# Kernel tuning notes

Hardware: AMD Instinct MI355X
Metric: run time of the kernel (lower is better)

## Reference

```python
import jax, jax.numpy as jnp
import numpy as np
from jax import lax

EPS = 1e-08


def setup_inputs() -> dict:
    key = jax.random.key(0)
    kX, kY, kXs, kW, kA, kB1, kB2 = jax.random.split(key, 7)
    P, D, K, M = 8192, 1024, 131072, 512
    return {
        "X": jax.random.normal(kX, (P, D), dtype=jnp.float32),
        "y": jax.random.normal(kY, (P,), dtype=jnp.float32),
        "X_star": jax.random.normal(kXs, (K, D), dtype=jnp.float32),
        "gamma": jnp.float32(0.001),
        "W": jax.random.normal(kW, (M, D), dtype=jnp.float32) * 0.01,
        "a": jax.random.normal(kA, (M,), dtype=jnp.float32) * 0.01,
        "b1": jax.random.normal(kB1, (M,), dtype=jnp.float32) * 0.01,
        "b2": jnp.float32(0.1),
        "L": 64,
    }


def reference(X, y, X_star, gamma, W, a, b1, b2, L):
    P, D = X.shape
    Sigma_hat = (X.T @ X) / P                      # (D, D)
    I = jnp.eye(D, dtype=X.dtype)
    M_mat = I - (gamma / L) * Sigma_hat            # (D, D)

    # S = sum_{l=0}^{L-1} M^l, built sequentially as in the original loop
    def step(carry, _):
        S, Mp = carry
        return (S + Mp, Mp @ M_mat), None

    (S, _), _ = lax.scan(step, (jnp.zeros_like(I), I), None, length=L)

    rep = gamma * (S @ (X.T @ y))                  # (D,)
    linear_pred = (X_star @ rep) / (L * P)         # (K,)

    rep_normalized = rep / (jnp.linalg.norm(rep) + EPS)
    phi = X_star * rep_normalized                  # (K, D) elementwise
    hidden = jax.nn.relu(phi @ W.T + b1)           # (K, m)
    mlp_correction = hidden @ a                    # (K,)
    return linear_pred + mlp_correction + b2
```

## Files before the change

kernel.cpp:

```cpp
#include <hip/hip_runtime.h>
#include <hip/hip_bf16.h>
#include <stdint.h>

#define D_DIM 1024
#define P_ROWS 8192
#define K_ROWS 131072
#define M_DIM 512
#define L_STEPS 64
#define BM 128
#define XS_ROW_BYTES 4096

typedef short bf16x8_t __attribute__((ext_vector_type(8)));
typedef float f32x4_t __attribute__((ext_vector_type(4)));

typedef const __attribute__((address_space(1))) void* gas_t;
typedef __attribute__((address_space(3))) void* las_t;

__device__ __forceinline__ uint32_t f2bf(float f) {
  union { float f; uint32_t u; } c; c.f = f;
  const uint32_t u = c.u;
  return (u + 0x7FFFu + ((u >> 16) & 1u)) >> 16;
}

__device__ __forceinline__ bf16x8_t as_bf16x8(uint4 v) {
  union { uint4 u; bf16x8_t h; } c; c.u = v; return c.h;
}

__device__ __forceinline__ bf16x8_t cvt_frag(const f32x4_t& a0, const f32x4_t& a1) {
  uint32_t p0, p1, p2, p3;
  asm("v_cvt_pk_bf16_f32 %0, %1, %2" : "=v"(p0) : "v"(a0[0]), "v"(a0[1]));
  asm("v_cvt_pk_bf16_f32 %0, %1, %2" : "=v"(p1) : "v"(a0[2]), "v"(a0[3]));
  asm("v_cvt_pk_bf16_f32 %0, %1, %2" : "=v"(p2) : "v"(a1[0]), "v"(a1[1]));
  asm("v_cvt_pk_bf16_f32 %0, %1, %2" : "=v"(p3) : "v"(a1[2]), "v"(a1[3]));
  union { uint32_t u[4]; bf16x8_t h; } c;
  c.u[0] = p0; c.u[1] = p1; c.u[2] = p2; c.u[3] = p3;
  return c.h;
}

__global__ void xty_kernel(const float* __restrict__ X, const float* __restrict__ y,
                           float* __restrict__ v) {
  const int d0 = threadIdx.x * 4;
  float a0 = 0.f, a1 = 0.f, a2 = 0.f, a3 = 0.f;
  for (int i = blockIdx.x; i < P_ROWS; i += gridDim.x) {
    const float s = y[i];
    const float4 x = *reinterpret_cast<const float4*>(X + (size_t)i * D_DIM + d0);
    a0 += s * x.x; a1 += s * x.y; a2 += s * x.z; a3 += s * x.w;
  }
  atomicAdd(v + d0 + 0, a0);
  atomicAdd(v + d0 + 1, a1);
  atomicAdd(v + d0 + 2, a2);
  atomicAdd(v + d0 + 3, a3);
}

__global__ void xtxw_kernel(const float* __restrict__ X, const float* __restrict__ win,
                            float* __restrict__ wout) {
  __shared__ float red[4][D_DIM];
  const int lane = threadIdx.x & 63;
  const int wave = threadIdx.x >> 6;
  const int gw = blockIdx.x * 4 + wave;
  const int nw = gridDim.x * 4;
  float wv[16], acc[16];
#pragma unroll
  for (int q = 0; q < 4; ++q) {
    const float4 tv = *reinterpret_cast<const float4*>(win + q * 256 + lane * 4);
    wv[q*4+0] = tv.x; wv[q*4+1] = tv.y; wv[q*4+2] = tv.z; wv[q*4+3] = tv.w;
  }
#pragma unroll
  for (int j = 0; j < 16; ++j) acc[j] = 0.f;
  for (int i = gw; i < P_ROWS; i += nw) {
    const float* xr = X + (size_t)i * D_DIM;
    float xv[16];
    float dot = 0.f;
#pragma unroll
    for (int q = 0; q < 4; ++q) {
      const float4 tv = *reinterpret_cast<const float4*>(xr + q * 256 + lane * 4);
      xv[q*4+0] = tv.x; xv[q*4+1] = tv.y; xv[q*4+2] = tv.z; xv[q*4+3] = tv.w;
      dot += tv.x * wv[q*4+0] + tv.y * wv[q*4+1] + tv.z * wv[q*4+2] + tv.w * wv[q*4+3];
    }
#pragma unroll
    for (int m = 1; m < 64; m <<= 1) dot += __shfl_xor(dot, m);
#pragma unroll
    for (int j = 0; j < 16; ++j) acc[j] += dot * xv[j];
  }
#pragma unroll
  for (int q = 0; q < 4; ++q) {
    float4 tv;
    tv.x = acc[q*4+0]; tv.y = acc[q*4+1]; tv.z = acc[q*4+2]; tv.w = acc[q*4+3];
    *reinterpret_cast<float4*>(&red[wave][q * 256 + lane * 4]) = tv;
  }
  __syncthreads();
  const int d0 = threadIdx.x * 4;
#pragma unroll
  for (int j = 0; j < 4; ++j)
    atomicAdd(wout + d0 + j, red[0][d0+j] + red[1][d0+j] + red[2][d0+j] + red[3][d0+j]);
}

__global__ void combine_kernel(const float* __restrict__ v, const float* __restrict__ u1,
                               const float* __restrict__ u2, const float* __restrict__ gamma_p,
                               float* __restrict__ rep_lin, float* __restrict__ repn) {
  __shared__ float sred[4];
  const float gamma = *gamma_p;
  const float eps = gamma / (float)L_STEPS;
  const float c1 = 2016.0f * eps / (float)P_ROWS;
  const float c2 = 41664.0f * eps * eps / ((float)P_ROWS * (float)P_ROWS);
  const int d0 = threadIdx.x * 4;
  float r[4];
  float ss = 0.f;
#pragma unroll
  for (int j = 0; j < 4; ++j) {
    const float val = gamma * ((float)L_STEPS * v[d0+j] - c1 * u1[d0+j] + c2 * u2[d0+j]);
    r[j] = val;
    ss += val * val;
  }
#pragma unroll
  for (int m = 1; m < 64; m <<= 1) ss += __shfl_xor(ss, m);
  if ((threadIdx.x & 63) == 0) sred[threadIdx.x >> 6] = ss;
  __syncthreads();
  const float norm = sqrtf(sred[0] + sred[1] + sred[2] + sred[3]);
  const float inv_norm = 1.0f / (norm + 1e-8f);
  const float lin_s = 1.0f / ((float)L_STEPS * (float)P_ROWS);
#pragma unroll
  for (int j = 0; j < 4; ++j) {
    rep_lin[d0+j] = r[j] * lin_s;
    repn[d0+j]    = r[j] * inv_norm;
  }
}

__global__ void wn_frag_kernel(const float* __restrict__ W, const float* __restrict__ repn,
                               ushort* __restrict__ WnF) {
  const int gid = blockIdx.x * 256 + threadIdx.x;
  const int l = gid & 63;
  const int f = (gid >> 6) & 31;
  const int s = gid >> 11;
  const int m = f * 16 + (l & 15);
  const int d0 = s * 32 + ((l >> 4) << 3);
  const float4 w0 = *reinterpret_cast<const float4*>(W + (size_t)m * D_DIM + d0);
  const float4 w1 = *reinterpret_cast<const float4*>(W + (size_t)m * D_DIM + d0 + 4);
  const float4 r0 = *reinterpret_cast<const float4*>(repn + d0);
  const float4 r1 = *reinterpret_cast<const float4*>(repn + d0 + 4);
  uint4 o;
  o.x = f2bf(w0.x*r0.x) | (f2bf(w0.y*r0.y) << 16);
  o.y = f2bf(w0.z*r0.z) | (f2bf(w0.w*r0.w) << 16);
  o.z = f2bf(w1.x*r1.x) | (f2bf(w1.y*r1.y) << 16);
  o.w = f2bf(w1.z*r1.z) | (f2bf(w1.w*r1.w) << 16);
  *reinterpret_cast<uint4*>(WnF + (size_t)gid * 8) = o;
}

__global__ __launch_bounds__(512, 2)
void fused_kernel(const float* __restrict__ Xs, const ushort* __restrict__ WnF,
                  const float* __restrict__ rep_lin, const float* __restrict__ b1,
                  const float* __restrict__ aw, const float* __restrict__ b2p,
                  float* __restrict__ out) {
  __shared__ __align__(16) char Abuf[4][16384];
  __shared__ __align__(16) float repl[D_DIM];
  __shared__ float mlp_acc[BM];
  __shared__ float lin_acc[BM];

  const int t = threadIdx.x;
  const int lane = t & 63;
  const int wid = t >> 6;
  const int wm = wid >> 2;
  const int wn = wid & 3;
  const int fr = lane & 15;
  const int kg = lane >> 4;
  const size_t blockRow = (size_t)blockIdx.x * BM;

  const int sr0 = wid * 16 + (lane >> 3);
  const int sr1 = sr0 + 8;
  const char* gA0 = (const char*)Xs + (blockRow + (size_t)sr0) * XS_ROW_BYTES
                  + (size_t)(((lane & 7) ^ (sr0 & 7)) * 16);
  const char* gA1 = (const char*)Xs + (blockRow + (size_t)sr1) * XS_ROW_BYTES
                  + (size_t)(((lane & 7) ^ (sr1 & 7)) * 16);

  const char* gB = (const char*)WnF + (size_t)wn * 8192 + (size_t)lane * 16;

  const int fs = fr & 7;
  const int arow = (wm * 64 + fr) * 128;
  const int aoff0 = arow + (((kg * 2)     ^ fs) * 16);
  const int aoff1 = arow + (((kg * 2 + 1) ^ fs) * 16);
  const int roff = kg * 32;

  auto stage = [&](int tile) {
    char* d0 = &Abuf[0][0] + (size_t)((tile & 3) * 16384 + wid * 2048);
    __builtin_amdgcn_global_load_lds((gas_t)(gA0 + (size_t)tile * 128), (las_t)d0, 16, 0, 0);
    __builtin_amdgcn_global_load_lds((gas_t)(gA1 + (size_t)tile * 128), (las_t)(d0 + 1024), 16, 0, 0);
  };

  f32x4_t acc[4][8];
#pragma unroll
  for (int mi = 0; mi < 4; ++mi)
#pragma unroll
    for (int ni = 0; ni < 8; ++ni)
      acc[mi][ni] = f32x4_t{0.f, 0.f, 0.f, 0.f};
  float lin[4] = {0.f, 0.f, 0.f, 0.f};

  if (t < BM) mlp_acc[t] = 0.f;
  repl[t] = rep_lin[t];
  repl[t + 512] = rep_lin[t + 512];
  stage(0); stage(1); stage(2);
  asm volatile("s_waitcnt vmcnt(0)" ::: "memory");
  __syncthreads();

  for (int s = 0; s < 32; ++s) {
    const char* Ab = &Abuf[0][0] + (s & 3) * 16384;
    const char* gBs = gB + (size_t)s * 32768;
    uint4 Bv[8];
#pragma unroll
    for (int ni = 0; ni < 8; ++ni)
      Bv[ni] = *reinterpret_cast<const uint4*>(gBs + ni * 1024);
    if (s < 29) stage(s + 3);
    f32x4_t va[4], vb[4];
#pragma unroll
    for (int mi = 0; mi < 4; ++mi) {
      va[mi] = *reinterpret_cast<const f32x4_t*>(Ab + aoff0 + mi * 2048);
      vb[mi] = *reinterpret_cast<const f32x4_t*>(Ab + aoff1 + mi * 2048);
    }
    if (wn == 0) {
      const f32x4_t rp0 = *reinterpret_cast<const f32x4_t*>((const char*)repl + s * 128 + roff);
      const f32x4_t rp1 = *reinterpret_cast<const f32x4_t*>((const char*)repl + s * 128 + roff + 16);
#pragma unroll
      for (int mi = 0; mi < 4; ++mi)
        lin[mi] += va[mi][0]*rp0[0] + va[mi][1]*rp0[1] + va[mi][2]*rp0[2] + va[mi][3]*rp0[3]
                 + vb[mi][0]*rp1[0] + vb[mi][1]*rp1[1] + vb[mi][2]*rp1[2] + vb[mi][3]*rp1[3];
    }
    bf16x8_t afr[4];
#pragma unroll
    for (int mi = 0; mi < 4; ++mi)
      afr[mi] = cvt_frag(va[mi], vb[mi]);
    __builtin_amdgcn_sched_barrier(0);
    if (s < 29) { asm volatile("s_waitcnt vmcnt(2)" ::: "memory"); }
    else        { asm volatile("s_waitcnt vmcnt(0)" ::: "memory"); }
    __builtin_amdgcn_sched_barrier(0);
    __builtin_amdgcn_s_setprio(1);
#pragma unroll
    for (int mi = 0; mi < 4; ++mi)
#pragma unroll
      for (int ni = 0; ni < 8; ++ni)
        acc[mi][ni] = __builtin_amdgcn_mfma_f32_16x16x32_bf16(afr[mi], as_bf16x8(Bv[ni]), acc[mi][ni], 0, 0, 0);
    __builtin_amdgcn_s_setprio(0);
    __builtin_amdgcn_sched_barrier(0);
    __builtin_amdgcn_s_barrier();
  }

  float b1r[8], ar[8];
#pragma unroll
  for (int ni = 0; ni < 8; ++ni) {
    const int c = wn * 128 + ni * 16 + fr;
    b1r[ni] = b1[c];
    ar[ni]  = aw[c];
  }
#pragma unroll
  for (int mi = 0; mi < 4; ++mi) {
#pragma unroll
    for (int r = 0; r < 4; ++r) {
      float sum = 0.f;
#pragma unroll
      for (int ni = 0; ni < 8; ++ni) {
        const float h = acc[mi][ni][r] + b1r[ni];
        sum += fmaxf(h, 0.f) * ar[ni];
      }
      sum += __shfl_xor(sum, 1);
      sum += __shfl_xor(sum, 2);
      sum += __shfl_xor(sum, 4);
      sum += __shfl_xor(sum, 8);
      if (fr == 0) {
        const int row = wm * 64 + mi * 16 + kg * 4 + r;
        atomicAdd(&mlp_acc[row], sum);
      }
    }
  }
  if (wn == 0) {
#pragma unroll
    for (int mi = 0; mi < 4; ++mi) {
      lin[mi] += __shfl_xor(lin[mi], 16);
      lin[mi] += __shfl_xor(lin[mi], 32);
    }
    if (lane < 16) {
#pragma unroll
      for (int mi = 0; mi < 4; ++mi)
        lin_acc[wm * 64 + mi * 16 + lane] = lin[mi];
    }
  }
  __syncthreads();
  if (t < BM)
    out[blockRow + t] = lin_acc[t] + mlp_acc[t] + b2p[0];
}

extern "C" void kernel_launch(void* const* d_in, const int* in_sizes, int n_in,
                              void* d_out, int out_size, void* d_ws, size_t ws_size,
                              hipStream_t stream) {
  const float* X     = (const float*)d_in[0];
  const float* y     = (const float*)d_in[1];
  const float* Xs    = (const float*)d_in[2];
  const float* gamma = (const float*)d_in[3];
  const float* W     = (const float*)d_in[4];
  const float* a     = (const float*)d_in[5];
  const float* b1    = (const float*)d_in[6];
  const float* b2    = (const float*)d_in[7];
  float* out = (float*)d_out;

  char* ws = (char*)d_ws;
  float*  v       = (float*)(ws + 0);
  float*  u1      = (float*)(ws + 4096);
  float*  u2      = (float*)(ws + 8192);
  float*  rep_lin = (float*)(ws + 12288);
  float*  repn    = (float*)(ws + 16384);
  ushort* WnF     = (ushort*)(ws + 20480);

  hipMemsetAsync(ws, 0, 3 * 4096, stream);
  hipLaunchKernelGGL(xty_kernel,     dim3(256), dim3(256), 0, stream, X, y, v);
  hipLaunchKernelGGL(xtxw_kernel,    dim3(256), dim3(256), 0, stream, X, v, u1);
  hipLaunchKernelGGL(xtxw_kernel,    dim3(256), dim3(256), 0, stream, X, u1, u2);
  hipLaunchKernelGGL(combine_kernel, dim3(1),   dim3(256), 0, stream, v, u1, u2, gamma, rep_lin, repn);
  hipLaunchKernelGGL(wn_frag_kernel, dim3(256), dim3(256), 0, stream, W, repn, WnF);
  hipLaunchKernelGGL(fused_kernel,   dim3(K_ROWS / BM), dim3(512), 0, stream,
                     Xs, WnF, rep_lin, b1, a, b2, out);
}
```

Before: 359.2 us.

## Load X_star fragments directly from global memory instead of LDS staging

```diff
diff --git a/kernel.cpp b/kernel.cpp
--- a/kernel.cpp
+++ b/kernel.cpp
@@ -12,9 +12,6 @@
 
 typedef short bf16x8_t __attribute__((ext_vector_type(8)));
 typedef float f32x4_t __attribute__((ext_vector_type(4)));
-
-typedef const __attribute__((address_space(1))) void* gas_t;
-typedef __attribute__((address_space(3))) void* las_t;
 
 __device__ __forceinline__ uint32_t f2bf(float f) {
   union { float f; uint32_t u; } c; c.f = f;
@@ -151,8 +148,6 @@
                   const float* __restrict__ rep_lin, const float* __restrict__ b1,
                   const float* __restrict__ aw, const float* __restrict__ b2p,
                   float* __restrict__ out) {
-  __shared__ __align__(16) char Abuf[4][16384];
-  __shared__ __align__(16) float repl[D_DIM];
   __shared__ float mlp_acc[BM];
   __shared__ float lin_acc[BM];
 
@@ -165,26 +160,12 @@
   const int kg = lane >> 4;
   const size_t blockRow = (size_t)blockIdx.x * BM;
 
-  const int sr0 = wid * 16 + (lane >> 3);
-  const int sr1 = sr0 + 8;
-  const char* gA0 = (const char*)Xs + (blockRow + (size_t)sr0) * XS_ROW_BYTES
-                  + (size_t)(((lane & 7) ^ (sr0 & 7)) * 16);
-  const char* gA1 = (const char*)Xs + (blockRow + (size_t)sr1) * XS_ROW_BYTES
-                  + (size_t)(((lane & 7) ^ (sr1 & 7)) * 16);
-
-  const char* gB = (const char*)WnF + (size_t)wn * 8192 + (size_t)lane * 16;
-
-  const int fs = fr & 7;
-  const int arow = (wm * 64 + fr) * 128;
-  const int aoff0 = arow + (((kg * 2)     ^ fs) * 16);
-  const int aoff1 = arow + (((kg * 2 + 1) ^ fs) * 16);
-  const int roff = kg * 32;
-
-  auto stage = [&](int tile) {
-    char* d0 = &Abuf[0][0] + (size_t)((tile & 3) * 16384 + wid * 2048);
-    __builtin_amdgcn_global_load_lds((gas_t)(gA0 + (size_t)tile * 128), (las_t)d0, 16, 0, 0);
-    __builtin_amdgcn_global_load_lds((gas_t)(gA1 + (size_t)tile * 128), (las_t)(d0 + 1024), 16, 0, 0);
-  };
+  const char* gA = (const char*)Xs + (blockRow + (size_t)(wm * 64 + fr)) * XS_ROW_BYTES
+                 + (size_t)kg * 32;
+  const char* gB = (const char*)WnF + (size_t)(wn * 8) * 1024 + (size_t)lane * 16;
+  const char* gR = (const char*)rep_lin + (size_t)kg * 32;
+
+  if (t < BM) mlp_acc[t] = 0.f;
 
   f32x4_t acc[4][8];
 #pragma unroll
@@ -194,30 +175,22 @@
       acc[mi][ni] = f32x4_t{0.f, 0.f, 0.f, 0.f};
   float lin[4] = {0.f, 0.f, 0.f, 0.f};
 
-  if (t < BM) mlp_acc[t] = 0.f;
-  repl[t] = rep_lin[t];
-  repl[t + 512] = rep_lin[t + 512];
-  stage(0); stage(1); stage(2);
-  asm volatile("s_waitcnt vmcnt(0)" ::: "memory");
-  __syncthreads();
-
   for (int s = 0; s < 32; ++s) {
-    const char* Ab = &Abuf[0][0] + (s & 3) * 16384;
     const char* gBs = gB + (size_t)s * 32768;
+    const char* gAs = gA + (size_t)s * 128;
     uint4 Bv[8];
 #pragma unroll
     for (int ni = 0; ni < 8; ++ni)
       Bv[ni] = *reinterpret_cast<const uint4*>(gBs + ni * 1024);
-    if (s < 29) stage(s + 3);
     f32x4_t va[4], vb[4];
 #pragma unroll
     for (int mi = 0; mi < 4; ++mi) {
-      va[mi] = *reinterpret_cast<const f32x4_t*>(Ab + aoff0 + mi * 2048);
-      vb[mi] = *reinterpret_cast<const f32x4_t*>(Ab + aoff1 + mi * 2048);
+      va[mi] = *reinterpret_cast<const f32x4_t*>(gAs + mi * 65536);
+      vb[mi] = *reinterpret_cast<const f32x4_t*>(gAs + mi * 65536 + 16);
     }
     if (wn == 0) {
-      const f32x4_t rp0 = *reinterpret_cast<const f32x4_t*>((const char*)repl + s * 128 + roff);
-      const f32x4_t rp1 = *reinterpret_cast<const f32x4_t*>((const char*)repl + s * 128 + roff + 16);
+      const f32x4_t rp0 = *reinterpret_cast<const f32x4_t*>(gR + s * 128);
+      const f32x4_t rp1 = *reinterpret_cast<const f32x4_t*>(gR + s * 128 + 16);
 #pragma unroll
       for (int mi = 0; mi < 4; ++mi)
         lin[mi] += va[mi][0]*rp0[0] + va[mi][1]*rp0[1] + va[mi][2]*rp0[2] + va[mi][3]*rp0[3]
@@ -227,19 +200,11 @@
 #pragma unroll
     for (int mi = 0; mi < 4; ++mi)
       afr[mi] = cvt_frag(va[mi], vb[mi]);
-    __builtin_amdgcn_sched_barrier(0);
-    if (s < 29) { asm volatile("s_waitcnt vmcnt(2)" ::: "memory"); }
-    else        { asm volatile("s_waitcnt vmcnt(0)" ::: "memory"); }
-    __builtin_amdgcn_sched_barrier(0);
-    __builtin_amdgcn_s_setprio(1);
 #pragma unroll
     for (int mi = 0; mi < 4; ++mi)
 #pragma unroll
       for (int ni = 0; ni < 8; ++ni)
         acc[mi][ni] = __builtin_amdgcn_mfma_f32_16x16x32_bf16(afr[mi], as_bf16x8(Bv[ni]), acc[mi][ni], 0, 0, 0);
-    __builtin_amdgcn_s_setprio(0);
-    __builtin_amdgcn_sched_barrier(0);
-    __builtin_amdgcn_s_barrier();
   }
 
   float b1r[8], ar[8];
```

New measurement: 460.7 us. 1.28x slower.
